# Performance work log

Measured on AMD Instinct MI355X. Metric: run time of the kernel, lower is better.

Reference implementation:

```python
import jax, jax.numpy as jnp
import numpy as np

B, T, D = 4096, 200, 64
NEG_INF = -(2.0 ** 32) + 1.0  # matches tf paddings constant


def setup_inputs() -> dict:
    key = jax.random.key(0)
    ks = jax.random.split(key, 12)
    queries = jax.random.normal(ks[0], (B, D), dtype=jnp.float32)
    keys = jax.random.normal(ks[1], (B, T, D), dtype=jnp.float32)
    keys_length = jax.random.randint(ks[2], (B,), 0, 200, dtype=jnp.int32)
    # attention MLP params (glorot-ish scale)
    W1 = jax.random.normal(ks[3], (4 * D, 16), dtype=jnp.float32) * (1.0 / np.sqrt(4 * D))
    b1 = jnp.zeros((16,), dtype=jnp.float32)
    W2 = jax.random.normal(ks[4], (16, 8), dtype=jnp.float32) * (1.0 / np.sqrt(16))
    b2 = jnp.zeros((8,), dtype=jnp.float32)
    W3 = jax.random.normal(ks[5], (8, 1), dtype=jnp.float32) * (1.0 / np.sqrt(8))
    b3 = jnp.zeros((1,), dtype=jnp.float32)
    W4 = jax.random.normal(ks[6], (D, D), dtype=jnp.float32) * (1.0 / np.sqrt(D))
    b4 = jnp.zeros((D,), dtype=jnp.float32)
    return {"queries": queries, "keys": keys, "keys_length": keys_length,
            "W1": W1, "b1": b1, "W2": W2, "b2": b2, "W3": W3, "b3": b3,
            "W4": W4, "b4": b4}


def reference(queries, keys, keys_length, W1, b1, W2, b2, W3, b3, W4, b4):
    Bq, Tq, Dq = keys.shape
    # tile queries across time: [B, T, D]
    q = jnp.broadcast_to(queries[:, None, :], (Bq, Tq, Dq))
    # DIN feature construction: [B, T, 4D]
    din_all = jnp.concatenate([q, keys, q - keys, q * keys], axis=-1)
    # tiny MLP scorer
    x = jax.nn.sigmoid(jnp.einsum('btf,fh->bth', din_all, W1) + b1)
    x = jax.nn.sigmoid(jnp.einsum('bth,hk->btk', x, W2) + b2)
    scores = (jnp.einsum('btk,ko->bto', x, W3) + b3)[..., 0]  # [B, T]
    # mask invalid history positions
    mask = jnp.arange(Tq, dtype=keys_length.dtype)[None, :] < keys_length[:, None]
    scores = jnp.where(mask, scores, NEG_INF)
    scores = scores / (Dq ** 0.5)  # scaling applied after masking, as in tf code
    attn = jax.nn.softmax(scores, axis=-1)  # [B, T]
    out = jnp.einsum('bt,btd->bd', attn, keys)  # weighted sum of keys
    out = out @ W4 + b4  # [B, D]
    return out
```

## Files before the change

kernel.cpp:

```cpp
#include <hip/hip_runtime.h>
#include <math.h>

#define TT 200
#define MTS 72

typedef __attribute__((ext_vector_type(8))) short bf16x8;
typedef __attribute__((ext_vector_type(4))) float f32x4;

union BF8 { bf16x8 v; unsigned u[4]; };

__device__ __forceinline__ float sigmoidf_(float x) {
    return 1.0f / (1.0f + __expf(-x));
}
__device__ __forceinline__ unsigned cvtpk(float a, float b) {
    unsigned r;
    asm("v_cvt_pk_bf16_f32 %0, %1, %2" : "=v"(r) : "v"(a), "v"(b));
    return r;
}
__device__ __forceinline__ short f2bf(float x) {
    unsigned u = __float_as_uint(x);
    u += 0x7fff + ((u >> 16) & 1);
    return (short)(u >> 16);
}
__device__ __forceinline__ float bf2f(short s) {
    return __uint_as_float(((unsigned)(unsigned short)s) << 16);
}

__global__ __launch_bounds__(256, 4) void din_attn_flash(
    const float* __restrict__ queries,
    const float* __restrict__ keys,
    const int*   __restrict__ keys_length,
    const float* __restrict__ W1,
    const float* __restrict__ b1,
    const float* __restrict__ W2,
    const float* __restrict__ b2,
    const float* __restrict__ W3,
    const float* __restrict__ b3,
    const float* __restrict__ W4,
    const float* __restrict__ b4,
    float* __restrict__ out,
    int Bn)
{
    __shared__ __align__(16) short MtHi[4][16 * MTS];
    __shared__ __align__(16) short MtLo[4][16 * MTS];
    __shared__ __align__(16) float vS[4][64];

    const int tid  = threadIdx.x;
    const int w    = tid >> 6;
    const int lane = tid & 63;
    const int m16  = lane & 15;
    const int quad = lane >> 4;

    const int b = blockIdx.x * 4 + w;
    if (b >= Bn) return;
    const int len = __builtin_amdgcn_readfirstlane(keys_length[b]);
    const float* kb = keys + (size_t)b * (TT * 64);

    float cp0 = 0.f, cp1 = 0.f, cp2 = 0.f, cp3 = 0.f;
    {
        const int d2 = lane >> 2;
        const int hg = lane & 3;
        const float4* W1v = (const float4*)W1;
        #pragma unroll
        for (int dg = 0; dg < 4; dg++) {
            const int d = dg * 16 + d2;
            const float q = queries[b * 64 + d];
            float4 a  = W1v[(0   + d) * 4 + hg];
            float4 bb = W1v[(64  + d) * 4 + hg];
            float4 cc = W1v[(128 + d) * 4 + hg];
            float4 dd = W1v[(192 + d) * 4 + hg];
            float mv0 = bb.x - cc.x + q * dd.x;
            float mv1 = bb.y - cc.y + q * dd.y;
            float mv2 = bb.z - cc.z + q * dd.z;
            float mv3 = bb.w - cc.w + q * dd.w;
            cp0 += q * (a.x + cc.x);
            cp1 += q * (a.y + cc.y);
            cp2 += q * (a.z + cc.z);
            cp3 += q * (a.w + cc.w);
            const int hb = hg * 4;
            short h0 = f2bf(mv0), h1 = f2bf(mv1), h2 = f2bf(mv2), h3 = f2bf(mv3);
            MtHi[w][(hb + 0) * MTS + d] = h0;
            MtHi[w][(hb + 1) * MTS + d] = h1;
            MtHi[w][(hb + 2) * MTS + d] = h2;
            MtHi[w][(hb + 3) * MTS + d] = h3;
            MtLo[w][(hb + 0) * MTS + d] = f2bf(mv0 - bf2f(h0));
            MtLo[w][(hb + 1) * MTS + d] = f2bf(mv1 - bf2f(h1));
            MtLo[w][(hb + 2) * MTS + d] = f2bf(mv2 - bf2f(h2));
            MtLo[w][(hb + 3) * MTS + d] = f2bf(mv3 - bf2f(h3));
        }
        #pragma unroll
        for (int mask = 4; mask <= 32; mask <<= 1) {
            cp0 += __shfl_xor(cp0, mask, 64);
            cp1 += __shfl_xor(cp1, mask, 64);
            cp2 += __shfl_xor(cp2, mask, 64);
            cp3 += __shfl_xor(cp3, mask, 64);
        }
    }
    float cv4[4];
    cv4[0] = __shfl(cp0, quad, 64) + b1[quad * 4 + 0];
    cv4[1] = __shfl(cp1, quad, 64) + b1[quad * 4 + 1];
    cv4[2] = __shfl(cp2, quad, 64) + b1[quad * 4 + 2];
    cv4[3] = __shfl(cp3, quad, 64) + b1[quad * 4 + 3];

    asm volatile("" ::: "memory");
    __builtin_amdgcn_wave_barrier();

    const int bb0 = m16 * MTS + quad * 8;
    const bf16x8 Bh0 = *(const bf16x8*)&MtHi[w][bb0];
    const bf16x8 Bh1 = *(const bf16x8*)&MtHi[w][bb0 + 32];
    const bf16x8 Bl0 = *(const bf16x8*)&MtLo[w][bb0];
    const bf16x8 Bl1 = *(const bf16x8*)&MtLo[w][bb0 + 32];

    BF8 a2;
    {
        float w2f[4];
        #pragma unroll
        for (int j = 0; j < 4; j++)
            w2f[j] = (m16 < 8) ? W2[(quad * 4 + j) * 8 + m16] : 0.0f;
        a2.u[0] = cvtpk(w2f[0], w2f[1]);
        a2.u[1] = cvtpk(w2f[2], w2f[3]);
        a2.u[2] = 0u;
        a2.u[3] = 0u;
    }

    const float4 b2a = *(const float4*)(b2);
    const float4 b2b = *(const float4*)(b2 + 4);
    const float4 w3a = *(const float4*)(W3);
    const float4 w3b = *(const float4*)(W3 + 4);
    const float  b3v = b3[0];
    const float b2k0 = quad == 0 ? b2a.x : (quad == 1 ? b2b.x : 0.f);
    const float b2k1 = quad == 0 ? b2a.y : (quad == 1 ? b2b.y : 0.f);
    const float b2k2 = quad == 0 ? b2a.z : (quad == 1 ? b2b.z : 0.f);
    const float b2k3 = quad == 0 ? b2a.w : (quad == 1 ? b2b.w : 0.f);
    const float w3k0 = quad == 0 ? w3a.x : (quad == 1 ? w3b.x : 0.f);
    const float w3k1 = quad == 0 ? w3a.y : (quad == 1 ? w3b.y : 0.f);
    const float w3k2 = quad == 0 ? w3a.z : (quad == 1 ? w3b.z : 0.f);
    const float w3k3 = quad == 0 ? w3a.w : (quad == 1 ? w3b.w : 0.f);

    const float M = 0.125f * (fabsf(b3v)
                  + fabsf(w3a.x) + fabsf(w3a.y) + fabsf(w3a.z) + fabsf(w3a.w)
                  + fabsf(w3b.x) + fabsf(w3b.y) + fabsf(w3b.z) + fabsf(w3b.w));

    const int lenEff = (len == 0) ? TT : len;
    const int ntiles = (lenEff + 15) >> 4;

    float ssum = 0.0f;
    float o[16];
    #pragma unroll
    for (int j = 0; j < 16; j++) o[j] = 0.0f;

    const float4 z4 = {0.f, 0.f, 0.f, 0.f};
    #define LOADT(TL, A0, A1, A2, A3)                                   \
        { const int t_ = (TL) * 16 + m16;                               \
          if (t_ < lenEff) {                                            \
              const float* p_ = kb + t_ * 64 + quad * 8;                \
              A0 = *(const float4*)(p_);                                \
              A1 = *(const float4*)(p_ + 4);                            \
              A2 = *(const float4*)(p_ + 32);                           \
              A3 = *(const float4*)(p_ + 36);                           \
          } else { A0 = z4; A1 = z4; A2 = z4; A3 = z4; } }

    float4 c0, c1, c2, c3, n0, n1, n2, n3;
    LOADT(0, c0, c1, c2, c3);
    LOADT(1, n0, n1, n2, n3);

    for (int tile = 0; tile < ntiles; tile++) {
        float4 m0, m1, m2, m3;
        LOADT(tile + 2, m0, m1, m2, m3);

        BF8 ah0, ah1;
        ah0.u[0] = cvtpk(c0.x, c0.y);  ah0.u[1] = cvtpk(c0.z, c0.w);
        ah0.u[2] = cvtpk(c1.x, c1.y);  ah0.u[3] = cvtpk(c1.z, c1.w);
        ah1.u[0] = cvtpk(c2.x, c2.y);  ah1.u[1] = cvtpk(c2.z, c2.w);
        ah1.u[2] = cvtpk(c3.x, c3.y);  ah1.u[3] = cvtpk(c3.z, c3.w);

        f32x4 acc = {0.f, 0.f, 0.f, 0.f};
        acc = __builtin_amdgcn_mfma_f32_16x16x32_bf16(Bh0, ah0.v, acc, 0, 0, 0);
        acc = __builtin_amdgcn_mfma_f32_16x16x32_bf16(Bl0, ah0.v, acc, 0, 0, 0);
        acc = __builtin_amdgcn_mfma_f32_16x16x32_bf16(Bh1, ah1.v, acc, 0, 0, 0);
        acc = __builtin_amdgcn_mfma_f32_16x16x32_bf16(Bl1, ah1.v, acc, 0, 0, 0);

        const float h10 = sigmoidf_(acc[0] + cv4[0]);
        const float h11 = sigmoidf_(acc[1] + cv4[1]);
        const float h12 = sigmoidf_(acc[2] + cv4[2]);
        const float h13 = sigmoidf_(acc[3] + cv4[3]);
        BF8 hb;
        hb.u[0] = cvtpk(h10, h11);
        hb.u[1] = cvtpk(h12, h13);
        hb.u[2] = 0u;
        hb.u[3] = 0u;

        f32x4 acc2 = {0.f, 0.f, 0.f, 0.f};
        acc2 = __builtin_amdgcn_mfma_f32_16x16x32_bf16(a2.v, hb.v, acc2, 0, 0, 0);

        float s3p;
        s3p = sigmoidf_(acc2[0] + b2k0) * w3k0;
        s3p = fmaf(sigmoidf_(acc2[1] + b2k1), w3k1, s3p);
        s3p = fmaf(sigmoidf_(acc2[2] + b2k2), w3k2, s3p);
        s3p = fmaf(sigmoidf_(acc2[3] + b2k3), w3k3, s3p);
        s3p += __shfl_xor(s3p, 16, 64);
        s3p += __shfl_xor(s3p, 32, 64);

        const int tg = tile * 16 + m16;
        float sc = (len == 0) ? 0.0f : (s3p + b3v) * 0.125f;
        if (tg >= lenEff) sc = -1.0e30f;
        const float p = __expf(sc - M);

        ssum += p;
        o[0]  = fmaf(p, c0.x, o[0]);
        o[1]  = fmaf(p, c0.y, o[1]);
        o[2]  = fmaf(p, c0.z, o[2]);
        o[3]  = fmaf(p, c0.w, o[3]);
        o[4]  = fmaf(p, c1.x, o[4]);
        o[5]  = fmaf(p, c1.y, o[5]);
        o[6]  = fmaf(p, c1.z, o[6]);
        o[7]  = fmaf(p, c1.w, o[7]);
        o[8]  = fmaf(p, c2.x, o[8]);
        o[9]  = fmaf(p, c2.y, o[9]);
        o[10] = fmaf(p, c2.z, o[10]);
        o[11] = fmaf(p, c2.w, o[11]);
        o[12] = fmaf(p, c3.x, o[12]);
        o[13] = fmaf(p, c3.y, o[13]);
        o[14] = fmaf(p, c3.z, o[14]);
        o[15] = fmaf(p, c3.w, o[15]);

        c0 = n0; c1 = n1; c2 = n2; c3 = n3;
        n0 = m0; n1 = m1; n2 = m2; n3 = m3;
    }
    #undef LOADT

    #pragma unroll
    for (int mask = 1; mask <= 8; mask <<= 1) {
        ssum += __shfl_xor(ssum, mask, 64);
        #pragma unroll
        for (int j = 0; j < 16; j++) o[j] += __shfl_xor(o[j], mask, 64);
    }
    const float inv = 1.0f / ssum;
    if (m16 == 0) {
        #pragma unroll
        for (int j = 0; j < 8; j++) vS[w][quad * 8 + j]      = o[j] * inv;
        #pragma unroll
        for (int j = 0; j < 8; j++) vS[w][32 + quad * 8 + j] = o[8 + j] * inv;
    }
    asm volatile("" ::: "memory");
    __builtin_amdgcn_wave_barrier();

    float po = b4[lane];
    const float4* vS4 = (const float4*)&vS[w][0];
    #pragma unroll 4
    for (int d0 = 0; d0 < 16; d0++) {
        const float4 vv = vS4[d0];
        const float* w4p = W4 + d0 * 256 + lane;
        po = fmaf(vv.x, w4p[0],   po);
        po = fmaf(vv.y, w4p[64],  po);
        po = fmaf(vv.z, w4p[128], po);
        po = fmaf(vv.w, w4p[192], po);
    }
    out[(size_t)b * 64 + lane] = po;
}

extern "C" void kernel_launch(void* const* d_in, const int* in_sizes, int n_in,
                              void* d_out, int out_size, void* d_ws, size_t ws_size,
                              hipStream_t stream) {
    const float* queries     = (const float*)d_in[0];
    const float* keys        = (const float*)d_in[1];
    const int*   keys_length = (const int*)  d_in[2];
    const float* W1 = (const float*)d_in[3];
    const float* b1 = (const float*)d_in[4];
    const float* W2 = (const float*)d_in[5];
    const float* b2 = (const float*)d_in[6];
    const float* W3 = (const float*)d_in[7];
    const float* b3 = (const float*)d_in[8];
    const float* W4 = (const float*)d_in[9];
    const float* b4 = (const float*)d_in[10];
    float* out = (float*)d_out;

    const int Bn = in_sizes[2];
    const int blocks = (Bn + 3) >> 2;
    din_attn_flash<<<blocks, 256, 0, stream>>>(
        queries, keys, keys_length, W1, b1, W2, b2, W3, b3, W4, b4, out, Bn);
}
```

Baseline: 294.2 us.

## Add persistent waves with atomic work-stealing for variable-length rows

Launches a fixed 512-block grid in which each wave first handles one of the last 2048 rows statically, then claims the remaining rows through an atomic counter in workspace memory, zeroed by a memset before launch. The aim is to balance load, since per-row cost varies with keys_length, so long-tail waves no longer leave compute units idle. Launch bounds drop from 4 to 2 blocks per SIMD, which loosens the register limit. The trade-off is an extra memset launch, atomic contention, and possibly lower occupancy.

```diff
diff --git a/kernel.cpp b/kernel.cpp
--- a/kernel.cpp
+++ b/kernel.cpp
@@ -26,7 +26,7 @@
     return __uint_as_float(((unsigned)(unsigned short)s) << 16);
 }
 
-__global__ __launch_bounds__(256, 4) void din_attn_flash(
+__global__ __launch_bounds__(256, 2) void din_attn_flash(
     const float* __restrict__ queries,
     const float* __restrict__ keys,
     const int*   __restrict__ keys_length,
@@ -39,7 +39,7 @@
     const float* __restrict__ W4,
     const float* __restrict__ b4,
     float* __restrict__ out,
-    int Bn)
+    int Bn, int dynBase, int* __restrict__ cnt)
 {
     __shared__ __align__(16) short MtHi[4][16 * MTS];
     __shared__ __align__(16) short MtLo[4][16 * MTS];
@@ -50,66 +50,7 @@
     const int lane = tid & 63;
     const int m16  = lane & 15;
     const int quad = lane >> 4;
-
-    const int b = blockIdx.x * 4 + w;
-    if (b >= Bn) return;
-    const int len = __builtin_amdgcn_readfirstlane(keys_length[b]);
-    const float* kb = keys + (size_t)b * (TT * 64);
-
-    float cp0 = 0.f, cp1 = 0.f, cp2 = 0.f, cp3 = 0.f;
-    {
-        const int d2 = lane >> 2;
-        const int hg = lane & 3;
-        const float4* W1v = (const float4*)W1;
-        #pragma unroll
-        for (int dg = 0; dg < 4; dg++) {
-            const int d = dg * 16 + d2;
-            const float q = queries[b * 64 + d];
-            float4 a  = W1v[(0   + d) * 4 + hg];
-            float4 bb = W1v[(64  + d) * 4 + hg];
-            float4 cc = W1v[(128 + d) * 4 + hg];
-            float4 dd = W1v[(192 + d) * 4 + hg];
-            float mv0 = bb.x - cc.x + q * dd.x;
-            float mv1 = bb.y - cc.y + q * dd.y;
-            float mv2 = bb.z - cc.z + q * dd.z;
-            float mv3 = bb.w - cc.w + q * dd.w;
-            cp0 += q * (a.x + cc.x);
-            cp1 += q * (a.y + cc.y);
-            cp2 += q * (a.z + cc.z);
-            cp3 += q * (a.w + cc.w);
-            const int hb = hg * 4;
-            short h0 = f2bf(mv0), h1 = f2bf(mv1), h2 = f2bf(mv2), h3 = f2bf(mv3);
-            MtHi[w][(hb + 0) * MTS + d] = h0;
-            MtHi[w][(hb + 1) * MTS + d] = h1;
-            MtHi[w][(hb + 2) * MTS + d] = h2;
-            MtHi[w][(hb + 3) * MTS + d] = h3;
-            MtLo[w][(hb + 0) * MTS + d] = f2bf(mv0 - bf2f(h0));
-            MtLo[w][(hb + 1) * MTS + d] = f2bf(mv1 - bf2f(h1));
-            MtLo[w][(hb + 2) * MTS + d] = f2bf(mv2 - bf2f(h2));
-            MtLo[w][(hb + 3) * MTS + d] = f2bf(mv3 - bf2f(h3));
-        }
-        #pragma unroll
-        for (int mask = 4; mask <= 32; mask <<= 1) {
-            cp0 += __shfl_xor(cp0, mask, 64);
-            cp1 += __shfl_xor(cp1, mask, 64);
-            cp2 += __shfl_xor(cp2, mask, 64);
-            cp3 += __shfl_xor(cp3, mask, 64);
-        }
-    }
-    float cv4[4];
-    cv4[0] = __shfl(cp0, quad, 64) + b1[quad * 4 + 0];
-    cv4[1] = __shfl(cp1, quad, 64) + b1[quad * 4 + 1];
-    cv4[2] = __shfl(cp2, quad, 64) + b1[quad * 4 + 2];
-    cv4[3] = __shfl(cp3, quad, 64) + b1[quad * 4 + 3];
-
-    asm volatile("" ::: "memory");
-    __builtin_amdgcn_wave_barrier();
-
-    const int bb0 = m16 * MTS + quad * 8;
-    const bf16x8 Bh0 = *(const bf16x8*)&MtHi[w][bb0];
-    const bf16x8 Bh1 = *(const bf16x8*)&MtHi[w][bb0 + 32];
-    const bf16x8 Bl0 = *(const bf16x8*)&MtLo[w][bb0];
-    const bf16x8 Bl1 = *(const bf16x8*)&MtLo[w][bb0 + 32];
+    const int gwid = blockIdx.x * 4 + w;
 
     BF8 a2;
     {
@@ -122,7 +63,6 @@
         a2.u[2] = 0u;
         a2.u[3] = 0u;
     }
-
     const float4 b2a = *(const float4*)(b2);
     const float4 b2b = *(const float4*)(b2 + 4);
     const float4 w3a = *(const float4*)(W3);
@@ -136,127 +76,196 @@
     const float w3k1 = quad == 0 ? w3a.y : (quad == 1 ? w3b.y : 0.f);
     const float w3k2 = quad == 0 ? w3a.z : (quad == 1 ? w3b.z : 0.f);
     const float w3k3 = quad == 0 ? w3a.w : (quad == 1 ? w3b.w : 0.f);
-
     const float M = 0.125f * (fabsf(b3v)
                   + fabsf(w3a.x) + fabsf(w3a.y) + fabsf(w3a.z) + fabsf(w3a.w)
                   + fabsf(w3b.x) + fabsf(w3b.y) + fabsf(w3b.z) + fabsf(w3b.w));
 
-    const int lenEff = (len == 0) ? TT : len;
-    const int ntiles = (lenEff + 15) >> 4;
-
-    float ssum = 0.0f;
-    float o[16];
-    #pragma unroll
-    for (int j = 0; j < 16; j++) o[j] = 0.0f;
-
-    const float4 z4 = {0.f, 0.f, 0.f, 0.f};
-    #define LOADT(TL, A0, A1, A2, A3)                                   \
-        { const int t_ = (TL) * 16 + m16;                               \
-          if (t_ < lenEff) {                                            \
-              const float* p_ = kb + t_ * 64 + quad * 8;                \
-              A0 = *(const float4*)(p_);                                \
-              A1 = *(const float4*)(p_ + 4);                            \
-              A2 = *(const float4*)(p_ + 32);                           \
-              A3 = *(const float4*)(p_ + 36);                           \
-          } else { A0 = z4; A1 = z4; A2 = z4; A3 = z4; } }
-
-    float4 c0, c1, c2, c3, n0, n1, n2, n3;
-    LOADT(0, c0, c1, c2, c3);
-    LOADT(1, n0, n1, n2, n3);
-
-    for (int tile = 0; tile < ntiles; tile++) {
-        float4 m0, m1, m2, m3;
-        LOADT(tile + 2, m0, m1, m2, m3);
-
-        BF8 ah0, ah1;
-        ah0.u[0] = cvtpk(c0.x, c0.y);  ah0.u[1] = cvtpk(c0.z, c0.w);
-        ah0.u[2] = cvtpk(c1.x, c1.y);  ah0.u[3] = cvtpk(c1.z, c1.w);
-        ah1.u[0] = cvtpk(c2.x, c2.y);  ah1.u[1] = cvtpk(c2.z, c2.w);
-        ah1.u[2] = cvtpk(c3.x, c3.y);  ah1.u[3] = cvtpk(c3.z, c3.w);
-
-        f32x4 acc = {0.f, 0.f, 0.f, 0.f};
-        acc = __builtin_amdgcn_mfma_f32_16x16x32_bf16(Bh0, ah0.v, acc, 0, 0, 0);
-        acc = __builtin_amdgcn_mfma_f32_16x16x32_bf16(Bl0, ah0.v, acc, 0, 0, 0);
-        acc = __builtin_amdgcn_mfma_f32_16x16x32_bf16(Bh1, ah1.v, acc, 0, 0, 0);
-        acc = __builtin_amdgcn_mfma_f32_16x16x32_bf16(Bl1, ah1.v, acc, 0, 0, 0);
-
-        const float h10 = sigmoidf_(acc[0] + cv4[0]);
-        const float h11 = sigmoidf_(acc[1] + cv4[1]);
-        const float h12 = sigmoidf_(acc[2] + cv4[2]);
-        const float h13 = sigmoidf_(acc[3] + cv4[3]);
-        BF8 hb;
-        hb.u[0] = cvtpk(h10, h11);
-        hb.u[1] = cvtpk(h12, h13);
-        hb.u[2] = 0u;
-        hb.u[3] = 0u;
-
-        f32x4 acc2 = {0.f, 0.f, 0.f, 0.f};
-        acc2 = __builtin_amdgcn_mfma_f32_16x16x32_bf16(a2.v, hb.v, acc2, 0, 0, 0);
-
-        float s3p;
-        s3p = sigmoidf_(acc2[0] + b2k0) * w3k0;
-        s3p = fmaf(sigmoidf_(acc2[1] + b2k1), w3k1, s3p);
-        s3p = fmaf(sigmoidf_(acc2[2] + b2k2), w3k2, s3p);
-        s3p = fmaf(sigmoidf_(acc2[3] + b2k3), w3k3, s3p);
-        s3p += __shfl_xor(s3p, 16, 64);
-        s3p += __shfl_xor(s3p, 32, 64);
-
-        const int tg = tile * 16 + m16;
-        float sc = (len == 0) ? 0.0f : (s3p + b3v) * 0.125f;
-        if (tg >= lenEff) sc = -1.0e30f;
-        const float p = __expf(sc - M);
-
-        ssum += p;
-        o[0]  = fmaf(p, c0.x, o[0]);
-        o[1]  = fmaf(p, c0.y, o[1]);
-        o[2]  = fmaf(p, c0.z, o[2]);
-        o[3]  = fmaf(p, c0.w, o[3]);
-        o[4]  = fmaf(p, c1.x, o[4]);
-        o[5]  = fmaf(p, c1.y, o[5]);
-        o[6]  = fmaf(p, c1.z, o[6]);
-        o[7]  = fmaf(p, c1.w, o[7]);
-        o[8]  = fmaf(p, c2.x, o[8]);
-        o[9]  = fmaf(p, c2.y, o[9]);
-        o[10] = fmaf(p, c2.z, o[10]);
-        o[11] = fmaf(p, c2.w, o[11]);
-        o[12] = fmaf(p, c3.x, o[12]);
-        o[13] = fmaf(p, c3.y, o[13]);
-        o[14] = fmaf(p, c3.z, o[14]);
-        o[15] = fmaf(p, c3.w, o[15]);
-
-        c0 = n0; c1 = n1; c2 = n2; c3 = n3;
-        n0 = m0; n1 = m1; n2 = m2; n3 = m3;
+    int row = dynBase + gwid;
+    if (row >= Bn) row = -1;
+
+    while (row >= 0) {
+        const int b = row;
+        const int len = __builtin_amdgcn_readfirstlane(keys_length[b]);
+        const float* kb = keys + (size_t)b * (TT * 64);
+
+        float cp0 = 0.f, cp1 = 0.f, cp2 = 0.f, cp3 = 0.f;
+        {
+            const int d2 = lane >> 2;
+            const int hg = lane & 3;
+            const float4* W1v = (const float4*)W1;
+            #pragma unroll
+            for (int dg = 0; dg < 4; dg++) {
+                const int d = dg * 16 + d2;
+                const float q = queries[b * 64 + d];
+                float4 a  = W1v[(0   + d) * 4 + hg];
+                float4 bb = W1v[(64  + d) * 4 + hg];
+                float4 cc = W1v[(128 + d) * 4 + hg];
+                float4 dd = W1v[(192 + d) * 4 + hg];
+                float mv0 = bb.x - cc.x + q * dd.x;
+                float mv1 = bb.y - cc.y + q * dd.y;
+                float mv2 = bb.z - cc.z + q * dd.z;
+                float mv3 = bb.w - cc.w + q * dd.w;
+                cp0 += q * (a.x + cc.x);
+                cp1 += q * (a.y + cc.y);
+                cp2 += q * (a.z + cc.z);
+                cp3 += q * (a.w + cc.w);
+                const int hb = hg * 4;
+                short h0 = f2bf(mv0), h1 = f2bf(mv1), h2 = f2bf(mv2), h3 = f2bf(mv3);
+                MtHi[w][(hb + 0) * MTS + d] = h0;
+                MtHi[w][(hb + 1) * MTS + d] = h1;
+                MtHi[w][(hb + 2) * MTS + d] = h2;
+                MtHi[w][(hb + 3) * MTS + d] = h3;
+                MtLo[w][(hb + 0) * MTS + d] = f2bf(mv0 - bf2f(h0));
+                MtLo[w][(hb + 1) * MTS + d] = f2bf(mv1 - bf2f(h1));
+                MtLo[w][(hb + 2) * MTS + d] = f2bf(mv2 - bf2f(h2));
+                MtLo[w][(hb + 3) * MTS + d] = f2bf(mv3 - bf2f(h3));
+            }
+            #pragma unroll
+            for (int mask = 4; mask <= 32; mask <<= 1) {
+                cp0 += __shfl_xor(cp0, mask, 64);
+                cp1 += __shfl_xor(cp1, mask, 64);
+                cp2 += __shfl_xor(cp2, mask, 64);
+                cp3 += __shfl_xor(cp3, mask, 64);
+            }
+        }
+        float cv4[4];
+        cv4[0] = __shfl(cp0, quad, 64) + b1[quad * 4 + 0];
+        cv4[1] = __shfl(cp1, quad, 64) + b1[quad * 4 + 1];
+        cv4[2] = __shfl(cp2, quad, 64) + b1[quad * 4 + 2];
+        cv4[3] = __shfl(cp3, quad, 64) + b1[quad * 4 + 3];
+
+        asm volatile("" ::: "memory");
+        __builtin_amdgcn_wave_barrier();
+
+        const int bb0 = m16 * MTS + quad * 8;
+        const bf16x8 Bh0 = *(const bf16x8*)&MtHi[w][bb0];
+        const bf16x8 Bh1 = *(const bf16x8*)&MtHi[w][bb0 + 32];
+        const bf16x8 Bl0 = *(const bf16x8*)&MtLo[w][bb0];
+        const bf16x8 Bl1 = *(const bf16x8*)&MtLo[w][bb0 + 32];
+
+        const int lenEff = (len == 0) ? TT : len;
+        const int ntiles = (lenEff + 15) >> 4;
+
+        float ssum = 0.0f;
+        float o[16];
+        #pragma unroll
+        for (int j = 0; j < 16; j++) o[j] = 0.0f;
+
+        const float4 z4 = {0.f, 0.f, 0.f, 0.f};
+        #define LOADT(TL, A0, A1, A2, A3)                                   \
+            { const int t_ = (TL) * 16 + m16;                               \
+              if (t_ < lenEff) {                                            \
+                  const float* p_ = kb + t_ * 64 + quad * 8;                \
+                  A0 = *(const float4*)(p_);                                \
+                  A1 = *(const float4*)(p_ + 4);                            \
+                  A2 = *(const float4*)(p_ + 32);                           \
+                  A3 = *(const float4*)(p_ + 36);                           \
+              } else { A0 = z4; A1 = z4; A2 = z4; A3 = z4; } }
+
+        float4 c0, c1, c2, c3, n0, n1, n2, n3;
+        LOADT(0, c0, c1, c2, c3);
+        LOADT(1, n0, n1, n2, n3);
+
+        for (int tile = 0; tile < ntiles; tile++) {
+            float4 m0, m1, m2, m3;
+            LOADT(tile + 2, m0, m1, m2, m3);
+
+            BF8 ah0, ah1;
+            ah0.u[0] = cvtpk(c0.x, c0.y);  ah0.u[1] = cvtpk(c0.z, c0.w);
+            ah0.u[2] = cvtpk(c1.x, c1.y);  ah0.u[3] = cvtpk(c1.z, c1.w);
+            ah1.u[0] = cvtpk(c2.x, c2.y);  ah1.u[1] = cvtpk(c2.z, c2.w);
+            ah1.u[2] = cvtpk(c3.x, c3.y);  ah1.u[3] = cvtpk(c3.z, c3.w);
+
+            f32x4 acc = {0.f, 0.f, 0.f, 0.f};
+            acc = __builtin_amdgcn_mfma_f32_16x16x32_bf16(Bh0, ah0.v, acc, 0, 0, 0);
+            acc = __builtin_amdgcn_mfma_f32_16x16x32_bf16(Bl0, ah0.v, acc, 0, 0, 0);
+            acc = __builtin_amdgcn_mfma_f32_16x16x32_bf16(Bh1, ah1.v, acc, 0, 0, 0);
+            acc = __builtin_amdgcn_mfma_f32_16x16x32_bf16(Bl1, ah1.v, acc, 0, 0, 0);
+
+            const float h10 = sigmoidf_(acc[0] + cv4[0]);
+            const float h11 = sigmoidf_(acc[1] + cv4[1]);
+            const float h12 = sigmoidf_(acc[2] + cv4[2]);
+            const float h13 = sigmoidf_(acc[3] + cv4[3]);
+            BF8 hb;
+            hb.u[0] = cvtpk(h10, h11);
+            hb.u[1] = cvtpk(h12, h13);
+            hb.u[2] = 0u;
+            hb.u[3] = 0u;
+
+            f32x4 acc2 = {0.f, 0.f, 0.f, 0.f};
+            acc2 = __builtin_amdgcn_mfma_f32_16x16x32_bf16(a2.v, hb.v, acc2, 0, 0, 0);
+
+            float s3p;
+            s3p = sigmoidf_(acc2[0] + b2k0) * w3k0;
+            s3p = fmaf(sigmoidf_(acc2[1] + b2k1), w3k1, s3p);
+            s3p = fmaf(sigmoidf_(acc2[2] + b2k2), w3k2, s3p);
+            s3p = fmaf(sigmoidf_(acc2[3] + b2k3), w3k3, s3p);
+            s3p += __shfl_xor(s3p, 16, 64);
+            s3p += __shfl_xor(s3p, 32, 64);
+
+            const int tg = tile * 16 + m16;
+            float sc = (len == 0) ? 0.0f : (s3p + b3v) * 0.125f;
+            if (tg >= lenEff) sc = -1.0e30f;
+            const float p = __expf(sc - M);
+
+            ssum += p;
+            o[0]  = fmaf(p, c0.x, o[0]);
+            o[1]  = fmaf(p, c0.y, o[1]);
+            o[2]  = fmaf(p, c0.z, o[2]);
+            o[3]  = fmaf(p, c0.w, o[3]);
+            o[4]  = fmaf(p, c1.x, o[4]);
+            o[5]  = fmaf(p, c1.y, o[5]);
+            o[6]  = fmaf(p, c1.z, o[6]);
+            o[7]  = fmaf(p, c1.w, o[7]);
+            o[8]  = fmaf(p, c2.x, o[8]);
+            o[9]  = fmaf(p, c2.y, o[9]);
+            o[10] = fmaf(p, c2.z, o[10]);
+            o[11] = fmaf(p, c2.w, o[11]);
+            o[12] = fmaf(p, c3.x, o[12]);
+            o[13] = fmaf(p, c3.y, o[13]);
+            o[14] = fmaf(p, c3.z, o[14]);
+            o[15] = fmaf(p, c3.w, o[15]);
+
+            c0 = n0; c1 = n1; c2 = n2; c3 = n3;
+            n0 = m0; n1 = m1; n2 = m2; n3 = m3;
+        }
+        #undef LOADT
+
+        #pragma unroll
+        for (int mask = 1; mask <= 8; mask <<= 1) {
+            ssum += __shfl_xor(ssum, mask, 64);
+            #pragma unroll
+            for (int j = 0; j < 16; j++) o[j] += __shfl_xor(o[j], mask, 64);
+        }
+        const float inv = 1.0f / ssum;
+        if (m16 == 0) {
+            #pragma unroll
+            for (int j = 0; j < 8; j++) vS[w][quad * 8 + j]      = o[j] * inv;
+            #pragma unroll
+            for (int j = 0; j < 8; j++) vS[w][32 + quad * 8 + j] = o[8 + j] * inv;
+        }
+        asm volatile("" ::: "memory");
+        __builtin_amdgcn_wave_barrier();
+
+        float po = b4[lane];
+        const float4* vS4 = (const float4*)&vS[w][0];
+        #pragma unroll 4
+        for (int d0 = 0; d0 < 16; d0++) {
+            const float4 vv = vS4[d0];
+            const float* w4p = W4 + d0 * 256 + lane;
+            po = fmaf(vv.x, w4p[0],   po);
+            po = fmaf(vv.y, w4p[64],  po);
+            po = fmaf(vv.z, w4p[128], po);
+            po = fmaf(vv.w, w4p[192], po);
+        }
+        out[(size_t)b * 64 + lane] = po;
+
+        if (cnt == nullptr) break;
+        int r = 0;
+        if (lane == 0) r = atomicAdd(cnt, 1);
+        r = __shfl(r, 0, 64);
+        row = (r < dynBase) ? r : -1;
     }
-    #undef LOADT
-
-    #pragma unroll
-    for (int mask = 1; mask <= 8; mask <<= 1) {
-        ssum += __shfl_xor(ssum, mask, 64);
-        #pragma unroll
-        for (int j = 0; j < 16; j++) o[j] += __shfl_xor(o[j], mask, 64);
-    }
-    const float inv = 1.0f / ssum;
-    if (m16 == 0) {
-        #pragma unroll
-        for (int j = 0; j < 8; j++) vS[w][quad * 8 + j]      = o[j] * inv;
-        #pragma unroll
-        for (int j = 0; j < 8; j++) vS[w][32 + quad * 8 + j] = o[8 + j] * inv;
-    }
-    asm volatile("" ::: "memory");
-    __builtin_amdgcn_wave_barrier();
-
-    float po = b4[lane];
-    const float4* vS4 = (const float4*)&vS[w][0];
-    #pragma unroll 4
-    for (int d0 = 0; d0 < 16; d0++) {
-        const float4 vv = vS4[d0];
-        const float* w4p = W4 + d0 * 256 + lane;
-        po = fmaf(vv.x, w4p[0],   po);
-        po = fmaf(vv.y, w4p[64],  po);
-        po = fmaf(vv.z, w4p[128], po);
-        po = fmaf(vv.w, w4p[192], po);
-    }
-    out[(size_t)b * 64 + lane] = po;
 }
 
 extern "C" void kernel_launch(void* const* d_in, const int* in_sizes, int n_in,
@@ -276,7 +285,18 @@
     float* out = (float*)d_out;
 
     const int Bn = in_sizes[2];
-    const int blocks = (Bn + 3) >> 2;
+    int* cnt = nullptr;
+    int blocks, dynBase;
+    if (ws_size >= sizeof(int) && Bn > 2048) {
+        blocks  = 512;
+        dynBase = Bn - 2048;
+        cnt     = (int*)d_ws;
+        hipMemsetAsync(cnt, 0, sizeof(int), stream);
+    } else {
+        blocks  = (Bn + 3) >> 2;
+        dynBase = 0;
+    }
     din_attn_flash<<<blocks, 256, 0, stream>>>(
-        queries, keys, keys_length, W1, b1, W2, b2, W3, b3, W4, b4, out, Bn);
-}
+        queries, keys, keys_length, W1, b1, W2, b2, W3, b3, W4, b4, out,
+        Bn, dynBase, cnt);
+}
```

After: 307.0 us. 4.3% more time.
